# Kernel optimization log

Measured on AMD Instinct MI355X. Metric: run time of the kernel, lower is better.

Reference implementation:

```python
import jax, jax.numpy as jnp
import numpy as np

LN_EPS = 1e-5


def _sage_mean(x, Wl, bl, src, dst, ew, n_nodes):
    # lin_l then gather-weight-scatter mean: out[i] = mean_{j->i} ew * (x[j] @ Wl + bl)
    h = x @ Wl + bl                                  # [N, D]
    msg = h[src] * ew[:, None]                       # [E, D] gather + scale
    s = jax.ops.segment_sum(msg, dst, num_segments=n_nodes)          # [N, D]
    cnt = jax.ops.segment_sum(jnp.ones_like(ew), dst, num_segments=n_nodes)
    return s / jnp.maximum(cnt, 1.0)[:, None]


def _layernorm(x, gamma, beta):
    mu = jnp.mean(x, axis=-1, keepdims=True)
    var = jnp.var(x, axis=-1, keepdims=True)
    return (x - mu) * jax.lax.rsqrt(var + LN_EPS) * gamma + beta


def setup_inputs() -> dict:
    key = jax.random.key(0)
    ks = jax.random.split(key, 8)
    N, E, D = 50000, 800000, 128
    x = jax.random.normal(ks[0], (N, D), dtype=jnp.float32)
    edge_index = jax.random.randint(ks[1], (2, E), 0, N, dtype=jnp.int64)
    edge_weight = jax.random.uniform(ks[2], (E,), dtype=jnp.float32)
    sc = 1.0 / np.sqrt(D)
    Wl1 = jax.random.normal(ks[3], (D, D), dtype=jnp.float32) * sc
    bl1 = jnp.zeros((D,), dtype=jnp.float32)
    Wl2 = jax.random.normal(ks[4], (D, D), dtype=jnp.float32) * sc
    bl2 = jnp.zeros((D,), dtype=jnp.float32)
    gamma = jnp.ones((D,), dtype=jnp.float32)
    beta = jnp.zeros((D,), dtype=jnp.float32)
    return {"x": x, "edge_index": edge_index, "edge_weight": edge_weight,
            "Wl1": Wl1, "bl1": bl1, "Wl2": Wl2, "bl2": bl2,
            "gamma": gamma, "beta": beta}


def reference(x, edge_index, edge_weight, Wl1, bl1, Wl2, bl2, gamma, beta):
    N = x.shape[0]
    src, dst = edge_index[0], edge_index[1]
    # Layer 1: WeightedSAGEConv (no self-loops; update() returns aggr only)
    x1 = _sage_mean(x, Wl1, bl1, src, dst, edge_weight, N)
    # Layer 2: ResGraphConv — residual is Identity (in==out), add self-loops w=1
    loops = jnp.arange(N, dtype=edge_index.dtype)
    src2 = jnp.concatenate([src, loops])
    dst2 = jnp.concatenate([dst, loops])
    ew2 = jnp.concatenate([edge_weight, jnp.ones((N,), dtype=edge_weight.dtype)])
    out = _sage_mean(x1, Wl2, bl2, src2, dst2, ew2, N)
    out = _layernorm(out + x1, gamma, beta)
    return jax.nn.gelu(out, approximate=False)
```

## Files before the change

### kernel.cpp

```cpp
#include <hip/hip_runtime.h>
#include <math.h>

#define DF 128
#define NPB 256
#define EPB 4096
#define EPBA 2048
#define CAP 7168

typedef __attribute__((ext_vector_type(8))) short bf16x8;
typedef __attribute__((ext_vector_type(4))) float f32x4;

__device__ __forceinline__ float bf2f(uint u) {
    union { uint i; float f; } v; v.i = u << 16; return v.f;
}
__device__ __forceinline__ uint f2bf(float f) {
    union { float f; uint i; } v; v.f = f;
    return (v.i + 0x7fffu + ((v.i >> 16) & 1u)) >> 16;
}


__global__ void prep_k(const float* __restrict__ x, uint* __restrict__ xb, int n4,
                       const float* __restrict__ W1, const float* __restrict__ W2,
                       uint* __restrict__ Wt1, uint* __restrict__ Wt2,
                       const int* __restrict__ dst, int* __restrict__ bhist, int E,
                       int cvtxB) {
    __shared__ int lh[256];
    int b = blockIdx.x;
    int t = threadIdx.x;
    if (b < cvtxB) {
        int i = b * 256 + t;
        if (i < n4) {
            float4 v = ((const float4*)x)[i];
            uint2 o;
            o.x = f2bf(v.x) | (f2bf(v.y) << 16);
            o.y = f2bf(v.z) | (f2bf(v.w) << 16);
            ((uint2*)xb)[i] = o;
        }
    } else if (b < cvtxB + 64) {
        int i = (b - cvtxB) * 256 + t;
        const float* W = (i < 8192) ? W1 : W2;
        uint* Wt = (i < 8192) ? Wt1 : Wt2;
        int j = i & 8191;
        int n = j >> 6, kk = j & 63;
        Wt[n * 64 + kk] = f2bf(W[(2 * kk) * DF + n]) | (f2bf(W[(2 * kk + 1) * DF + n]) << 16);
    } else {
        int hb = b - cvtxB - 64;
        int base = hb * EPB;
        lh[t] = 0;
        __syncthreads();
#pragma unroll
        for (int k = 0; k < EPB / 256; ++k) {
            int i = base + k * 256 + t;
            if (i < E) atomicAdd(&lh[dst[i] >> 8], 1);
        }
        __syncthreads();
        bhist[hb * 256 + t] = lh[t];
    }
}

__global__ void bscan_k(const int* __restrict__ bhist, int histB,
                        int* __restrict__ bkoff, int* __restrict__ gcur) {
    int t = threadIdx.x;
    int v = 0;
#pragma unroll 4
    for (int hb = 0; hb < histB; ++hb) v += bhist[hb * 256 + t];
    __shared__ int sm[256];
    sm[t] = v;
    __syncthreads();
    for (int off = 1; off < 256; off <<= 1) {
        int u = (t >= off) ? sm[t - off] : 0;
        __syncthreads();
        sm[t] += u;
        __syncthreads();
    }
    int ex = sm[t] - v;
    bkoff[t] = ex;
    gcur[t] = ex;
    if (t == 255) bkoff[256] = sm[255];
}

__global__ __launch_bounds__(256) void passA_k(
    const int* __restrict__ src, const int* __restrict__ dst,
    const float* __restrict__ ew, int* __restrict__ gcur,
    uint2* __restrict__ stage, int E) {
    __shared__ int lhist[256];
    __shared__ int lscan[256];
    __shared__ int lcur[256];
    __shared__ int gbase[256];
    __shared__ int lbk[EPBA];
    __shared__ uint2 img[EPBA];
    int t = threadIdx.x;
    int base = blockIdx.x * EPBA;
    int cnt = min(EPBA, E - base);
    lhist[t] = 0;
    __syncthreads();
    uint ps[EPBA / 256], pw[EPBA / 256];
    int pb[EPBA / 256];
#pragma unroll
    for (int k = 0; k < EPBA / 256; ++k) {
        int i = base + k * 256 + t;
        pb[k] = -1;
        if (i < E) {
            int d = dst[i];
            int bk = d >> 8;
            pb[k] = bk;
            ps[k] = (uint)src[i] | ((uint)(d & 255) << 23);
            pw[k] = __float_as_uint(ew[i]);
            atomicAdd(&lhist[bk], 1);
        }
    }
    __syncthreads();
    int v = lhist[t];
    lscan[t] = v;
    __syncthreads();
    for (int off = 1; off < 256; off <<= 1) {
        int u = (t >= off) ? lscan[t - off] : 0;
        __syncthreads();
        lscan[t] += u;
        __syncthreads();
    }
    lcur[t] = lscan[t] - v;
    if (v > 0) gbase[t] = atomicAdd(&gcur[t], v);
    __syncthreads();
#pragma unroll
    for (int k = 0; k < EPBA / 256; ++k) {
        if (pb[k] >= 0) {
            int p = atomicAdd(&lcur[pb[k]], 1);
            img[p] = make_uint2(ps[k], pw[k]);
            lbk[p] = pb[k];
        }
    }
    __syncthreads();
    for (int i = t; i < cnt; i += 256) {
        int bk = lbk[i];
        stage[gbase[bk] + (i - (lscan[bk] - lhist[bk]))] = img[i];
    }
}

__global__ __launch_bounds__(256) void passB_k(
    const uint2* __restrict__ stage, const int* __restrict__ bkoff,
    int* __restrict__ rowptr, int* __restrict__ cursor,
    int2* __restrict__ adj, int N, int nbk) {
    __shared__ int lhist[256];
    __shared__ int lpre[256];
    __shared__ int lcur[256];
    __shared__ uint2 img[CAP];
    int t = threadIdx.x;
    int b = blockIdx.x;
    int nb0 = b * NPB;
    int nn = min(NPB, N - nb0);
    int ebase = bkoff[b];
    int ecnt = bkoff[b + 1] - ebase;
    lhist[t] = 0;
    __syncthreads();
    for (int i = t; i < ecnt; i += 256) {
        uint2 e = stage[ebase + i];
        atomicAdd(&lhist[(e.x >> 23) & 255], 1);
    }
    __syncthreads();
    int v = lhist[t];
    lpre[t] = v;
    __syncthreads();
    for (int off = 1; off < 256; off <<= 1) {
        int u = (t >= off) ? lpre[t - off] : 0;
        __syncthreads();
        lpre[t] += u;
        __syncthreads();
    }
    int myoff = lpre[t] - v;
    lcur[t] = myoff;
    if (t < nn) {
        rowptr[nb0 + t] = ebase + myoff;
        cursor[nb0 + t] = ebase + myoff;
    }
    if (b == nbk - 1 && t == 0) rowptr[N] = ebase + ecnt;
    __syncthreads();
    if (ecnt <= CAP) {
        for (int i = t; i < ecnt; i += 256) {
            uint2 e = stage[ebase + i];
            int p = atomicAdd(&lcur[(e.x >> 23) & 255], 1);
            img[p] = make_uint2(e.x & 0x7fffffu, e.y);
        }
        __syncthreads();
        for (int i = t; i < ecnt; i += 256) {
            uint2 e = img[i];
            adj[ebase + i] = make_int2((int)e.x, (int)e.y);
        }
    } else {
        for (int i = t; i < ecnt; i += 256) {
            uint2 e = stage[ebase + i];
            int dl = (e.x >> 23) & 255;
            int p = atomicAdd(&cursor[nb0 + dl], 1);
            adj[p] = make_int2((int)(e.x & 0x7fffffu), (int)e.y);
        }
    }
}


__global__ void histn_k(const int* __restrict__ dst, int* __restrict__ cnt, int E) {
    int i = blockIdx.x * blockDim.x + threadIdx.x;
    if (i < E) atomicAdd(&cnt[dst[i]], 1);
}

__global__ void partial_k(const int* __restrict__ cnt, int* __restrict__ bsum, int N) {
    int t = threadIdx.x, b = blockIdx.x;
    int base = b * 1024 + t * 4;
    int s = 0;
    if (base + 4 <= N) {
        int4 v = *(const int4*)(cnt + base);
        s = v.x + v.y + v.z + v.w;
    } else {
        for (int j = 0; j < 4; ++j)
            if (base + j < N) s += cnt[base + j];
    }
    __shared__ int sm[256];
    sm[t] = s;
    __syncthreads();
    for (int off = 128; off > 0; off >>= 1) {
        if (t < off) sm[t] += sm[t + off];
        __syncthreads();
    }
    if (t == 0) bsum[b] = sm[0];
}

__global__ void scanb_k(const int* __restrict__ bsum, int* __restrict__ boff,
                        int* __restrict__ rowptr, int nb, int N) {
    int t = threadIdx.x;
    int v = (t < nb) ? bsum[t] : 0;
    __shared__ int sm[256];
    sm[t] = v;
    __syncthreads();
    for (int off = 1; off < 256; off <<= 1) {
        int u = (t >= off) ? sm[t - off] : 0;
        __syncthreads();
        sm[t] += u;
        __syncthreads();
    }
    if (t < nb) boff[t] = sm[t] - v;
    if (t == 255) rowptr[N] = sm[255];
}

__global__ void rowfill_k(const int* __restrict__ cnt, const int* __restrict__ boff,
                          int* __restrict__ rowptr, int* __restrict__ cursor, int N) {
    int t = threadIdx.x, b = blockIdx.x;
    int base = b * 1024 + t * 4;
    int c0 = 0, c1 = 0, c2 = 0, c3 = 0;
    if (base + 4 <= N) {
        int4 v = *(const int4*)(cnt + base);
        c0 = v.x; c1 = v.y; c2 = v.z; c3 = v.w;
    } else {
        if (base + 0 < N) c0 = cnt[base + 0];
        if (base + 1 < N) c1 = cnt[base + 1];
        if (base + 2 < N) c2 = cnt[base + 2];
        if (base + 3 < N) c3 = cnt[base + 3];
    }
    int s = c0 + c1 + c2 + c3;
    __shared__ int sm[256];
    sm[t] = s;
    __syncthreads();
    for (int off = 1; off < 256; off <<= 1) {
        int u = (t >= off) ? sm[t - off] : 0;
        __syncthreads();
        sm[t] += u;
        __syncthreads();
    }
    int run = boff[b] + sm[t] - s;
    if (base + 0 < N) { rowptr[base + 0] = run; cursor[base + 0] = run; run += c0; }
    if (base + 1 < N) { rowptr[base + 1] = run; cursor[base + 1] = run; run += c1; }
    if (base + 2 < N) { rowptr[base + 2] = run; cursor[base + 2] = run; run += c2; }
    if (base + 3 < N) { rowptr[base + 3] = run; cursor[base + 3] = run; run += c3; }
}

__global__ void fill_k(const int* __restrict__ src, const int* __restrict__ dst,
                       const float* __restrict__ ew, int* __restrict__ cursor,
                       int2* __restrict__ adj, int E) {
    int i = blockIdx.x * blockDim.x + threadIdx.x;
    if (i < E) {
        int p = atomicAdd(&cursor[dst[i]], 1);
        int2 e;
        e.x = src[i];
        e.y = __float_as_int(ew[i]);
        adj[p] = e;
    }
}


template <int SELF>
__global__ void agg_k(const uint4* __restrict__ xb4, const int* __restrict__ rowptr,
                      const int2* __restrict__ adj, uint4* __restrict__ aggb4,
                      float* __restrict__ sumew, int N) {
    int wid = (blockIdx.x * blockDim.x + threadIdx.x) >> 6;
    int lane = threadIdx.x & 63;
    if (wid >= N) return;
    int g = lane >> 4;
    int c = lane & 15;
    int lo = rowptr[wid], hi = rowptr[wid + 1];
    float a0 = 0.f, a1 = 0.f, a2 = 0.f, a3 = 0.f;
    float a4 = 0.f, a5 = 0.f, a6 = 0.f, a7 = 0.f, ws = 0.f;
    if (SELF && g == 0) {
        uint4 v = xb4[(size_t)wid * 16 + c];
        a0 = bf2f(v.x & 0xffffu); a1 = bf2f(v.x >> 16);
        a2 = bf2f(v.y & 0xffffu); a3 = bf2f(v.y >> 16);
        a4 = bf2f(v.z & 0xffffu); a5 = bf2f(v.z >> 16);
        a6 = bf2f(v.w & 0xffffu); a7 = bf2f(v.w >> 16);
    }
#define FMA8(V, W)                                                     \
    do {                                                               \
        a0 += (W) * bf2f((V).x & 0xffffu); a1 += (W) * bf2f((V).x >> 16); \
        a2 += (W) * bf2f((V).y & 0xffffu); a3 += (W) * bf2f((V).y >> 16); \
        a4 += (W) * bf2f((V).z & 0xffffu); a5 += (W) * bf2f((V).z >> 16); \
        a6 += (W) * bf2f((V).w & 0xffffu); a7 += (W) * bf2f((V).w >> 16); \
    } while (0)
    for (int base = lo; base < hi; base += 64) {
        int p = base + lane;
        int sidx = 0; float wv = 0.f;
        if (p < hi) {
            int2 e = adj[p];
            sidx = e.x;
            wv = __int_as_float(e.y);
        }
        ws += wv;
        int cnt = min(hi - base, 64);
        int j = 0;
        for (; j + 16 <= cnt; j += 16) {
            int s0 = __shfl(sidx, j + g),      s1 = __shfl(sidx, j + 4 + g);
            int s2 = __shfl(sidx, j + 8 + g),  s3 = __shfl(sidx, j + 12 + g);
            float w0 = __shfl(wv, j + g),      w1 = __shfl(wv, j + 4 + g);
            float w2 = __shfl(wv, j + 8 + g),  w3 = __shfl(wv, j + 12 + g);
            uint4 v0 = xb4[(size_t)s0 * 16 + c];
            uint4 v1 = xb4[(size_t)s1 * 16 + c];
            uint4 v2 = xb4[(size_t)s2 * 16 + c];
            uint4 v3 = xb4[(size_t)s3 * 16 + c];
            FMA8(v0, w0); FMA8(v1, w1); FMA8(v2, w2); FMA8(v3, w3);
        }
        for (; j < cnt; j += 4) {
            int s0 = __shfl(sidx, j + g);
            float w0 = __shfl(wv, j + g);
            uint4 v0 = xb4[(size_t)s0 * 16 + c];
            FMA8(v0, w0);
        }
    }
#undef FMA8
    a0 += __shfl_xor(a0, 16); a0 += __shfl_xor(a0, 32);
    a1 += __shfl_xor(a1, 16); a1 += __shfl_xor(a1, 32);
    a2 += __shfl_xor(a2, 16); a2 += __shfl_xor(a2, 32);
    a3 += __shfl_xor(a3, 16); a3 += __shfl_xor(a3, 32);
    a4 += __shfl_xor(a4, 16); a4 += __shfl_xor(a4, 32);
    a5 += __shfl_xor(a5, 16); a5 += __shfl_xor(a5, 32);
    a6 += __shfl_xor(a6, 16); a6 += __shfl_xor(a6, 32);
    a7 += __shfl_xor(a7, 16); a7 += __shfl_xor(a7, 32);
    if (!SELF) {
        ws += __shfl_xor(ws, 1);
        ws += __shfl_xor(ws, 2);
        ws += __shfl_xor(ws, 4);
        ws += __shfl_xor(ws, 8);
        ws += __shfl_xor(ws, 16);
        ws += __shfl_xor(ws, 32);
        if (lane == 0) sumew[wid] = ws;
    }
    float inv = SELF ? 1.0f / (float)(hi - lo + 1)
                     : 1.0f / fmaxf((float)(hi - lo), 1.0f);
    if (g == 0) {
        uint4 o;
        o.x = f2bf(a0 * inv) | (f2bf(a1 * inv) << 16);
        o.y = f2bf(a2 * inv) | (f2bf(a3 * inv) << 16);
        o.z = f2bf(a4 * inv) | (f2bf(a5 * inv) << 16);
        o.w = f2bf(a6 * inv) | (f2bf(a7 * inv) << 16);
        aggb4[(size_t)wid * 16 + c] = o;
    }
}


__global__ __launch_bounds__(256) void mm1_k(
    const ushort* __restrict__ aggb, const ushort* __restrict__ Wt,
    const float* __restrict__ bl, const float* __restrict__ sumew,
    const int* __restrict__ rowptr, ushort* __restrict__ x1b, int N) {
    int lane = threadIdx.x & 63;
    int strip = blockIdx.x * 4 + (threadIdx.x >> 6);
    int nstrips = (N + 15) >> 4;
    if (strip >= nstrips) return;
    int row0 = strip << 4;
    int arow = row0 + (lane & 15);
    if (arow >= N) arow = N - 1;
    int kg = (lane >> 4) << 3;
    int bcol = lane & 15;

    bf16x8 af[4];
#pragma unroll
    for (int kc = 0; kc < 4; ++kc)
        af[kc] = *(const bf16x8*)(aggb + (size_t)arow * DF + kc * 32 + kg);

    f32x4 acc[8];
#pragma unroll
    for (int nt = 0; nt < 8; ++nt) {
        f32x4 a = {0.f, 0.f, 0.f, 0.f};
#pragma unroll
        for (int kc = 0; kc < 4; ++kc) {
            bf16x8 bf = *(const bf16x8*)(Wt + (size_t)(nt * 16 + bcol) * DF + kc * 32 + kg);
            a = __builtin_amdgcn_mfma_f32_16x16x32_bf16(af[kc], bf, a, 0, 0, 0);
        }
        acc[nt] = a;
    }

#pragma unroll
    for (int r = 0; r < 4; ++r) {
        int R = row0 + ((lane >> 4) << 2) + r;
        if (R >= N) continue;
        int deg = rowptr[R + 1] - rowptr[R];
        float wb = sumew[R] / fmaxf((float)deg, 1.0f);
#pragma unroll
        for (int nt = 0; nt < 8; ++nt) {
            int col = nt * 16 + bcol;
            x1b[(size_t)R * DF + col] = (ushort)f2bf(acc[nt][r] + bl[col] * wb);
        }
    }
}

__device__ __forceinline__ float gelu_exact(float v) {
    return 0.5f * v * (1.0f + erff(v * 0.70710678118654752440f));
}

__global__ __launch_bounds__(256) void mm2_k(
    const ushort* __restrict__ aggb, const ushort* __restrict__ Wt,
    const float* __restrict__ bl, const float* __restrict__ sumew,
    const int* __restrict__ rowptr, const ushort* __restrict__ x1b,
    const float* __restrict__ gamma, const float* __restrict__ beta,
    float* __restrict__ out, int N) {
    int lane = threadIdx.x & 63;
    int strip = blockIdx.x * 4 + (threadIdx.x >> 6);
    int nstrips = (N + 15) >> 4;
    if (strip >= nstrips) return;
    int row0 = strip << 4;
    int arow = row0 + (lane & 15);
    if (arow >= N) arow = N - 1;
    int kg = (lane >> 4) << 3;
    int bcol = lane & 15;

    bf16x8 af[4];
#pragma unroll
    for (int kc = 0; kc < 4; ++kc)
        af[kc] = *(const bf16x8*)(aggb + (size_t)arow * DF + kc * 32 + kg);

    f32x4 acc[8];
#pragma unroll
    for (int nt = 0; nt < 8; ++nt) {
        f32x4 a = {0.f, 0.f, 0.f, 0.f};
#pragma unroll
        for (int kc = 0; kc < 4; ++kc) {
            bf16x8 bf = *(const bf16x8*)(Wt + (size_t)(nt * 16 + bcol) * DF + kc * 32 + kg);
            a = __builtin_amdgcn_mfma_f32_16x16x32_bf16(af[kc], bf, a, 0, 0, 0);
        }
        acc[nt] = a;
    }

#pragma unroll
    for (int r = 0; r < 4; ++r) {
        int R = row0 + ((lane >> 4) << 2) + r;
        if (R >= N) continue;
        int deg = rowptr[R + 1] - rowptr[R];
        float wb = (sumew[R] + 1.0f) / (float)(deg + 1);
        float pre[8];
        float s = 0.f;
#pragma unroll
        for (int nt = 0; nt < 8; ++nt) {
            int col = nt * 16 + bcol;
            pre[nt] = acc[nt][r] + bl[col] * wb + bf2f(x1b[(size_t)R * DF + col]);
            s += pre[nt];
        }
        s += __shfl_xor(s, 1);
        s += __shfl_xor(s, 2);
        s += __shfl_xor(s, 4);
        s += __shfl_xor(s, 8);
        float mu = s * (1.0f / 128.0f);
        float vs = 0.f;
#pragma unroll
        for (int nt = 0; nt < 8; ++nt) {
            float d = pre[nt] - mu;
            vs += d * d;
        }
        vs += __shfl_xor(vs, 1);
        vs += __shfl_xor(vs, 2);
        vs += __shfl_xor(vs, 4);
        vs += __shfl_xor(vs, 8);
        float rstd = rsqrtf(vs * (1.0f / 128.0f) + 1e-5f);
#pragma unroll
        for (int nt = 0; nt < 8; ++nt) {
            int col = nt * 16 + bcol;
            float y = (pre[nt] - mu) * rstd * gamma[col] + beta[col];
            out[(size_t)R * DF + col] = gelu_exact(y);
        }
    }
}


extern "C" void kernel_launch(void* const* d_in, const int* in_sizes, int n_in,
                              void* d_out, int out_size, void* d_ws, size_t ws_size,
                              hipStream_t stream) {
    const float* x     = (const float*)d_in[0];
    const int*   ei    = (const int*)d_in[1];
    const float* ew    = (const float*)d_in[2];
    const float* Wl1   = (const float*)d_in[3];
    const float* bl1   = (const float*)d_in[4];
    const float* Wl2   = (const float*)d_in[5];
    const float* bl2   = (const float*)d_in[6];
    const float* gamma = (const float*)d_in[7];
    const float* beta  = (const float*)d_in[8];
    float* out = (float*)d_out;

    int N = in_sizes[0] / DF;
    int E = in_sizes[2];
    const int* src = ei;
    const int* dst = ei + E;

    char* ws = (char*)d_ws;
    size_t off = 0;
    auto alloc = [&](size_t bytes) -> void* {
        void* p = ws + off;
        off += (bytes + 255) & ~(size_t)255;
        return p;
    };
    int histB = (E + EPB - 1) / EPB;
    float*  sumew   = (float*)alloc((size_t)N * 4);
    int*    rowptr  = (int*)alloc((size_t)(N + 1) * 4);
    int*    cursor  = (int*)alloc((size_t)N * 4);
    int*    bhist   = (int*)alloc((size_t)histB * 256 * 4);
    int*    bkoff   = (int*)alloc(1040);
    int*    gcur    = (int*)alloc(1024);
    int*    bsum    = (int*)alloc(1024);
    int*    boff    = (int*)alloc(1024);
    int2*   adj     = (int2*)alloc((size_t)E * 8);
    uint2*  stage   = (uint2*)alloc((size_t)E * 8);
    uint*   xb      = (uint*)alloc((size_t)N * DF * 2);
    uint*   aggb    = (uint*)alloc((size_t)N * DF * 2);
    ushort* x1b     = (ushort*)alloc((size_t)N * DF * 2);
    uint*   Wt1     = (uint*)alloc((size_t)DF * DF * 2);
    uint*   Wt2     = (uint*)alloc((size_t)DF * DF * 2);
    int*    cnt     = (int*)alloc((size_t)N * 4);

    int nbk = (N + NPB - 1) / NPB;
    int n4 = N * DF / 4;
    int cvtxB = (n4 + 255) / 256;

    if (nbk <= 256) {
        hipLaunchKernelGGL(prep_k, dim3(cvtxB + 64 + histB), dim3(256), 0, stream,
                           x, xb, n4, Wl1, Wl2, Wt1, Wt2, dst, bhist, E, cvtxB);
        hipLaunchKernelGGL(bscan_k, dim3(1), dim3(256), 0, stream, bhist, histB, bkoff, gcur);
        int aB = (E + EPBA - 1) / EPBA;
        hipLaunchKernelGGL(passA_k, dim3(aB), dim3(256), 0, stream, src, dst, ew, gcur, stage, E);
        hipLaunchKernelGGL(passB_k, dim3(nbk), dim3(256), 0, stream,
                           stage, bkoff, rowptr, cursor, adj, N, nbk);
    } else {
        hipMemsetAsync(cnt, 0, (size_t)N * 4, stream);
        hipLaunchKernelGGL(prep_k, dim3(cvtxB + 64), dim3(256), 0, stream,
                           x, xb, n4, Wl1, Wl2, Wt1, Wt2, dst, bhist, 0, cvtxB);
        int eb = (E + 255) / 256;
        hipLaunchKernelGGL(histn_k, dim3(eb), dim3(256), 0, stream, dst, cnt, E);
        int nb_scan = (N + 1023) / 1024;
        hipLaunchKernelGGL(partial_k, dim3(nb_scan), dim3(256), 0, stream, cnt, bsum, N);
        hipLaunchKernelGGL(scanb_k, dim3(1), dim3(256), 0, stream, bsum, boff, rowptr, nb_scan, N);
        hipLaunchKernelGGL(rowfill_k, dim3(nb_scan), dim3(256), 0, stream, cnt, boff, rowptr, cursor, N);
        hipLaunchKernelGGL(fill_k, dim3(eb), dim3(256), 0, stream, src, dst, ew, cursor, adj, E);
    }

    int nb = (N * 64 + 255) / 256;
    int nstrips = (N + 15) / 16;
    int mb = (nstrips + 3) / 4;

    hipLaunchKernelGGL(agg_k<0>, dim3(nb), dim3(256), 0, stream,
                       (const uint4*)xb, rowptr, adj, (uint4*)aggb, sumew, N);
    hipLaunchKernelGGL(mm1_k, dim3(mb), dim3(256), 0, stream,
                       (const ushort*)aggb, (const ushort*)Wt1, bl1, sumew, rowptr, x1b, N);
    hipLaunchKernelGGL(agg_k<1>, dim3(nb), dim3(256), 0, stream,
                       (const uint4*)x1b, rowptr, adj, (uint4*)aggb, sumew, N);
    hipLaunchKernelGGL(mm2_k, dim3(mb), dim3(256), 0, stream,
                       (const ushort*)aggb, (const ushort*)Wt2, bl2, sumew, rowptr, x1b, gamma, beta, out, N);
}
```

Baseline: 169.5 us.

## Fuse neighbor aggregation with MFMA projection into one kernel per layer

Merges the aggregation and matmul kernels for each layer into a single kernel. Each block aggregates 16 nodes into shared memory, then one wave runs the MFMA projection plus bias, and for layer 2 the residual, layernorm and GELU. This drops the intermediate aggregate buffer round-trip, the sumew array and two launches. In exchange, three of four waves sit idle during the matmul phase and Wt is reloaded per 16-row block.

```diff
diff --git a/kernel.cpp b/kernel.cpp
--- a/kernel.cpp
+++ b/kernel.cpp
@@ -79,6 +79,7 @@
     if (t == 255) bkoff[256] = sm[255];
 }
 
+
 __global__ __launch_bounds__(256) void passA_k(
     const int* __restrict__ src, const int* __restrict__ dst,
     const float* __restrict__ ew, int* __restrict__ gcur,
@@ -285,110 +286,122 @@
 }
 
 
+__device__ __forceinline__ float gelu_exact(float v) {
+    return 0.5f * v * (1.0f + erff(v * 0.70710678118654752440f));
+}
+
 template <int SELF>
-__global__ void agg_k(const uint4* __restrict__ xb4, const int* __restrict__ rowptr,
-                      const int2* __restrict__ adj, uint4* __restrict__ aggb4,
-                      float* __restrict__ sumew, int N) {
-    int wid = (blockIdx.x * blockDim.x + threadIdx.x) >> 6;
-    int lane = threadIdx.x & 63;
-    if (wid >= N) return;
-    int g = lane >> 4;
-    int c = lane & 15;
-    int lo = rowptr[wid], hi = rowptr[wid + 1];
-    float a0 = 0.f, a1 = 0.f, a2 = 0.f, a3 = 0.f;
-    float a4 = 0.f, a5 = 0.f, a6 = 0.f, a7 = 0.f, ws = 0.f;
-    if (SELF && g == 0) {
-        uint4 v = xb4[(size_t)wid * 16 + c];
-        a0 = bf2f(v.x & 0xffffu); a1 = bf2f(v.x >> 16);
-        a2 = bf2f(v.y & 0xffffu); a3 = bf2f(v.y >> 16);
-        a4 = bf2f(v.z & 0xffffu); a5 = bf2f(v.z >> 16);
-        a6 = bf2f(v.w & 0xffffu); a7 = bf2f(v.w >> 16);
-    }
-#define FMA8(V, W)                                                     \
-    do {                                                               \
+__global__ __launch_bounds__(256) void aggmm_k(
+    const uint4* __restrict__ xin4, const int* __restrict__ rowptr,
+    const int2* __restrict__ adj, const ushort* __restrict__ Wt,
+    const float* __restrict__ bl, const float* __restrict__ gamma,
+    const float* __restrict__ beta, ushort* __restrict__ outb,
+    float* __restrict__ outf, int N) {
+    __shared__ __align__(16) ushort rows[16][136];
+    __shared__ float wbs[16];
+    int t = threadIdx.x;
+    int wv = t >> 6;
+    int lane = t & 63;
+    int row0 = blockIdx.x << 4;
+    int g = lane >> 4, c = lane & 15;
+
+#define FMA8(V, W)                                                        \
+    do {                                                                  \
         a0 += (W) * bf2f((V).x & 0xffffu); a1 += (W) * bf2f((V).x >> 16); \
         a2 += (W) * bf2f((V).y & 0xffffu); a3 += (W) * bf2f((V).y >> 16); \
         a4 += (W) * bf2f((V).z & 0xffffu); a5 += (W) * bf2f((V).z >> 16); \
         a6 += (W) * bf2f((V).w & 0xffffu); a7 += (W) * bf2f((V).w >> 16); \
     } while (0)
-    for (int base = lo; base < hi; base += 64) {
-        int p = base + lane;
-        int sidx = 0; float wv = 0.f;
-        if (p < hi) {
-            int2 e = adj[p];
-            sidx = e.x;
-            wv = __int_as_float(e.y);
-        }
-        ws += wv;
-        int cnt = min(hi - base, 64);
-        int j = 0;
-        for (; j + 16 <= cnt; j += 16) {
-            int s0 = __shfl(sidx, j + g),      s1 = __shfl(sidx, j + 4 + g);
-            int s2 = __shfl(sidx, j + 8 + g),  s3 = __shfl(sidx, j + 12 + g);
-            float w0 = __shfl(wv, j + g),      w1 = __shfl(wv, j + 4 + g);
-            float w2 = __shfl(wv, j + 8 + g),  w3 = __shfl(wv, j + 12 + g);
-            uint4 v0 = xb4[(size_t)s0 * 16 + c];
-            uint4 v1 = xb4[(size_t)s1 * 16 + c];
-            uint4 v2 = xb4[(size_t)s2 * 16 + c];
-            uint4 v3 = xb4[(size_t)s3 * 16 + c];
-            FMA8(v0, w0); FMA8(v1, w1); FMA8(v2, w2); FMA8(v3, w3);
-        }
-        for (; j < cnt; j += 4) {
-            int s0 = __shfl(sidx, j + g);
-            float w0 = __shfl(wv, j + g);
-            uint4 v0 = xb4[(size_t)s0 * 16 + c];
-            FMA8(v0, w0);
-        }
-    }
-#undef FMA8
-    a0 += __shfl_xor(a0, 16); a0 += __shfl_xor(a0, 32);
-    a1 += __shfl_xor(a1, 16); a1 += __shfl_xor(a1, 32);
-    a2 += __shfl_xor(a2, 16); a2 += __shfl_xor(a2, 32);
-    a3 += __shfl_xor(a3, 16); a3 += __shfl_xor(a3, 32);
-    a4 += __shfl_xor(a4, 16); a4 += __shfl_xor(a4, 32);
-    a5 += __shfl_xor(a5, 16); a5 += __shfl_xor(a5, 32);
-    a6 += __shfl_xor(a6, 16); a6 += __shfl_xor(a6, 32);
-    a7 += __shfl_xor(a7, 16); a7 += __shfl_xor(a7, 32);
-    if (!SELF) {
+
+    for (int q = 0; q < 4; ++q) {
+        int i = wv + q * 4;
+        int node = row0 + i;
+        float a0 = 0.f, a1 = 0.f, a2 = 0.f, a3 = 0.f;
+        float a4 = 0.f, a5 = 0.f, a6 = 0.f, a7 = 0.f, ws = 0.f;
+        int lo = 0, hi = 0;
+        if (node < N) {
+            lo = rowptr[node];
+            hi = rowptr[node + 1];
+            if (SELF && g == 0) {
+                uint4 v = xin4[(size_t)node * 16 + c];
+                a0 = bf2f(v.x & 0xffffu); a1 = bf2f(v.x >> 16);
+                a2 = bf2f(v.y & 0xffffu); a3 = bf2f(v.y >> 16);
+                a4 = bf2f(v.z & 0xffffu); a5 = bf2f(v.z >> 16);
+                a6 = bf2f(v.w & 0xffffu); a7 = bf2f(v.w >> 16);
+            }
+        }
+        for (int base = lo; base < hi; base += 64) {
+            int p = base + lane;
+            int sidx = 0; float wv2 = 0.f;
+            if (p < hi) {
+                int2 e = adj[p];
+                sidx = e.x;
+                wv2 = __int_as_float(e.y);
+            }
+            ws += wv2;
+            int cnt = min(hi - base, 64);
+            int j = 0;
+            for (; j + 16 <= cnt; j += 16) {
+                int s0 = __shfl(sidx, j + g),     s1 = __shfl(sidx, j + 4 + g);
+                int s2 = __shfl(sidx, j + 8 + g), s3 = __shfl(sidx, j + 12 + g);
+                float w0 = __shfl(wv2, j + g),     w1 = __shfl(wv2, j + 4 + g);
+                float w2 = __shfl(wv2, j + 8 + g), w3 = __shfl(wv2, j + 12 + g);
+                uint4 v0 = xin4[(size_t)s0 * 16 + c];
+                uint4 v1 = xin4[(size_t)s1 * 16 + c];
+                uint4 v2 = xin4[(size_t)s2 * 16 + c];
+                uint4 v3 = xin4[(size_t)s3 * 16 + c];
+                FMA8(v0, w0); FMA8(v1, w1); FMA8(v2, w2); FMA8(v3, w3);
+            }
+            for (; j < cnt; j += 4) {
+                int s0 = __shfl(sidx, j + g);
+                float w0 = __shfl(wv2, j + g);
+                uint4 v0 = xin4[(size_t)s0 * 16 + c];
+                FMA8(v0, w0);
+            }
+        }
+        a0 += __shfl_xor(a0, 16); a0 += __shfl_xor(a0, 32);
+        a1 += __shfl_xor(a1, 16); a1 += __shfl_xor(a1, 32);
+        a2 += __shfl_xor(a2, 16); a2 += __shfl_xor(a2, 32);
+        a3 += __shfl_xor(a3, 16); a3 += __shfl_xor(a3, 32);
+        a4 += __shfl_xor(a4, 16); a4 += __shfl_xor(a4, 32);
+        a5 += __shfl_xor(a5, 16); a5 += __shfl_xor(a5, 32);
+        a6 += __shfl_xor(a6, 16); a6 += __shfl_xor(a6, 32);
+        a7 += __shfl_xor(a7, 16); a7 += __shfl_xor(a7, 32);
         ws += __shfl_xor(ws, 1);
         ws += __shfl_xor(ws, 2);
         ws += __shfl_xor(ws, 4);
         ws += __shfl_xor(ws, 8);
         ws += __shfl_xor(ws, 16);
         ws += __shfl_xor(ws, 32);
-        if (lane == 0) sumew[wid] = ws;
-    }
-    float inv = SELF ? 1.0f / (float)(hi - lo + 1)
-                     : 1.0f / fmaxf((float)(hi - lo), 1.0f);
-    if (g == 0) {
-        uint4 o;
-        o.x = f2bf(a0 * inv) | (f2bf(a1 * inv) << 16);
-        o.y = f2bf(a2 * inv) | (f2bf(a3 * inv) << 16);
-        o.z = f2bf(a4 * inv) | (f2bf(a5 * inv) << 16);
-        o.w = f2bf(a6 * inv) | (f2bf(a7 * inv) << 16);
-        aggb4[(size_t)wid * 16 + c] = o;
-    }
-}
-
-
-__global__ __launch_bounds__(256) void mm1_k(
-    const ushort* __restrict__ aggb, const ushort* __restrict__ Wt,
-    const float* __restrict__ bl, const float* __restrict__ sumew,
-    const int* __restrict__ rowptr, ushort* __restrict__ x1b, int N) {
-    int lane = threadIdx.x & 63;
-    int strip = blockIdx.x * 4 + (threadIdx.x >> 6);
-    int nstrips = (N + 15) >> 4;
-    if (strip >= nstrips) return;
-    int row0 = strip << 4;
-    int arow = row0 + (lane & 15);
-    if (arow >= N) arow = N - 1;
-    int kg = (lane >> 4) << 3;
-    int bcol = lane & 15;
-
+        int deg = hi - lo;
+        float inv, wb;
+        if (SELF) {
+            inv = 1.0f / (float)(deg + 1);
+            wb = (ws + 1.0f) * inv;
+        } else {
+            float dd = fmaxf((float)deg, 1.0f);
+            inv = 1.0f / dd;
+            wb = ws / dd;
+        }
+        if (g == 0) {
+            uint4 o;
+            o.x = f2bf(a0 * inv) | (f2bf(a1 * inv) << 16);
+            o.y = f2bf(a2 * inv) | (f2bf(a3 * inv) << 16);
+            o.z = f2bf(a4 * inv) | (f2bf(a5 * inv) << 16);
+            o.w = f2bf(a6 * inv) | (f2bf(a7 * inv) << 16);
+            *reinterpret_cast<uint4*>(&rows[i][c * 8]) = o;
+            if (c == 0) wbs[i] = wb;
+        }
+    }
+#undef FMA8
+    __syncthreads();
+    if (wv != 0) return;
+
+    int kg = g << 3;
     bf16x8 af[4];
 #pragma unroll
     for (int kc = 0; kc < 4; ++kc)
-        af[kc] = *(const bf16x8*)(aggb + (size_t)arow * DF + kc * 32 + kg);
+        af[kc] = *(const bf16x8*)&rows[c][kc * 32 + kg];
 
     f32x4 acc[8];
 #pragma unroll
@@ -396,98 +409,56 @@
         f32x4 a = {0.f, 0.f, 0.f, 0.f};
 #pragma unroll
         for (int kc = 0; kc < 4; ++kc) {
-            bf16x8 bf = *(const bf16x8*)(Wt + (size_t)(nt * 16 + bcol) * DF + kc * 32 + kg);
+            bf16x8 bf = *(const bf16x8*)(Wt + (size_t)(nt * 16 + c) * DF + kc * 32 + kg);
             a = __builtin_amdgcn_mfma_f32_16x16x32_bf16(af[kc], bf, a, 0, 0, 0);
         }
         acc[nt] = a;
     }
 
+    const ushort* xin_s = (const ushort*)xin4;
 #pragma unroll
     for (int r = 0; r < 4; ++r) {
-        int R = row0 + ((lane >> 4) << 2) + r;
+        int i = g * 4 + r;
+        int R = row0 + i;
         if (R >= N) continue;
-        int deg = rowptr[R + 1] - rowptr[R];
-        float wb = sumew[R] / fmaxf((float)deg, 1.0f);
-#pragma unroll
-        for (int nt = 0; nt < 8; ++nt) {
-            int col = nt * 16 + bcol;
-            x1b[(size_t)R * DF + col] = (ushort)f2bf(acc[nt][r] + bl[col] * wb);
-        }
-    }
-}
-
-__device__ __forceinline__ float gelu_exact(float v) {
-    return 0.5f * v * (1.0f + erff(v * 0.70710678118654752440f));
-}
-
-__global__ __launch_bounds__(256) void mm2_k(
-    const ushort* __restrict__ aggb, const ushort* __restrict__ Wt,
-    const float* __restrict__ bl, const float* __restrict__ sumew,
-    const int* __restrict__ rowptr, const ushort* __restrict__ x1b,
-    const float* __restrict__ gamma, const float* __restrict__ beta,
-    float* __restrict__ out, int N) {
-    int lane = threadIdx.x & 63;
-    int strip = blockIdx.x * 4 + (threadIdx.x >> 6);
-    int nstrips = (N + 15) >> 4;
-    if (strip >= nstrips) return;
-    int row0 = strip << 4;
-    int arow = row0 + (lane & 15);
-    if (arow >= N) arow = N - 1;
-    int kg = (lane >> 4) << 3;
-    int bcol = lane & 15;
-
-    bf16x8 af[4];
-#pragma unroll
-    for (int kc = 0; kc < 4; ++kc)
-        af[kc] = *(const bf16x8*)(aggb + (size_t)arow * DF + kc * 32 + kg);
-
-    f32x4 acc[8];
-#pragma unroll
-    for (int nt = 0; nt < 8; ++nt) {
-        f32x4 a = {0.f, 0.f, 0.f, 0.f};
-#pragma unroll
-        for (int kc = 0; kc < 4; ++kc) {
-            bf16x8 bf = *(const bf16x8*)(Wt + (size_t)(nt * 16 + bcol) * DF + kc * 32 + kg);
-            a = __builtin_amdgcn_mfma_f32_16x16x32_bf16(af[kc], bf, a, 0, 0, 0);
-        }
-        acc[nt] = a;
-    }
-
-#pragma unroll
-    for (int r = 0; r < 4; ++r) {
-        int R = row0 + ((lane >> 4) << 2) + r;
-        if (R >= N) continue;
-        int deg = rowptr[R + 1] - rowptr[R];
-        float wb = (sumew[R] + 1.0f) / (float)(deg + 1);
-        float pre[8];
-        float s = 0.f;
-#pragma unroll
-        for (int nt = 0; nt < 8; ++nt) {
-            int col = nt * 16 + bcol;
-            pre[nt] = acc[nt][r] + bl[col] * wb + bf2f(x1b[(size_t)R * DF + col]);
-            s += pre[nt];
-        }
-        s += __shfl_xor(s, 1);
-        s += __shfl_xor(s, 2);
-        s += __shfl_xor(s, 4);
-        s += __shfl_xor(s, 8);
-        float mu = s * (1.0f / 128.0f);
-        float vs = 0.f;
-#pragma unroll
-        for (int nt = 0; nt < 8; ++nt) {
-            float d = pre[nt] - mu;
-            vs += d * d;
-        }
-        vs += __shfl_xor(vs, 1);
-        vs += __shfl_xor(vs, 2);
-        vs += __shfl_xor(vs, 4);
-        vs += __shfl_xor(vs, 8);
-        float rstd = rsqrtf(vs * (1.0f / 128.0f) + 1e-5f);
-#pragma unroll
-        for (int nt = 0; nt < 8; ++nt) {
-            int col = nt * 16 + bcol;
-            float y = (pre[nt] - mu) * rstd * gamma[col] + beta[col];
-            out[(size_t)R * DF + col] = gelu_exact(y);
+        float wb = wbs[i];
+        if (!SELF) {
+#pragma unroll
+            for (int nt = 0; nt < 8; ++nt) {
+                int col = nt * 16 + c;
+                outb[(size_t)R * DF + col] = (ushort)f2bf(acc[nt][r] + bl[col] * wb);
+            }
+        } else {
+            float pre[8];
+            float s = 0.f;
+#pragma unroll
+            for (int nt = 0; nt < 8; ++nt) {
+                int col = nt * 16 + c;
+                pre[nt] = acc[nt][r] + bl[col] * wb + bf2f(xin_s[(size_t)R * DF + col]);
+                s += pre[nt];
+            }
+            s += __shfl_xor(s, 1);
+            s += __shfl_xor(s, 2);
+            s += __shfl_xor(s, 4);
+            s += __shfl_xor(s, 8);
+            float mu = s * (1.0f / 128.0f);
+            float vs = 0.f;
+#pragma unroll
+            for (int nt = 0; nt < 8; ++nt) {
+                float d = pre[nt] - mu;
+                vs += d * d;
+            }
+            vs += __shfl_xor(vs, 1);
+            vs += __shfl_xor(vs, 2);
+            vs += __shfl_xor(vs, 4);
+            vs += __shfl_xor(vs, 8);
+            float rstd = rsqrtf(vs * (1.0f / 128.0f) + 1e-5f);
+#pragma unroll
+            for (int nt = 0; nt < 8; ++nt) {
+                int col = nt * 16 + c;
+                float y = (pre[nt] - mu) * rstd * gamma[col] + beta[col];
+                outf[(size_t)R * DF + col] = gelu_exact(y);
+            }
         }
     }
 }
@@ -520,7 +491,6 @@
         return p;
     };
     int histB = (E + EPB - 1) / EPB;
-    float*  sumew   = (float*)alloc((size_t)N * 4);
     int*    rowptr  = (int*)alloc((size_t)(N + 1) * 4);
     int*    cursor  = (int*)alloc((size_t)N * 4);
     int*    bhist   = (int*)alloc((size_t)histB * 256 * 4);
@@ -531,7 +501,6 @@
     int2*   adj     = (int2*)alloc((size_t)E * 8);
     uint2*  stage   = (uint2*)alloc((size_t)E * 8);
     uint*   xb      = (uint*)alloc((size_t)N * DF * 2);
-    uint*   aggb    = (uint*)alloc((size_t)N * DF * 2);
     ushort* x1b     = (ushort*)alloc((size_t)N * DF * 2);
     uint*   Wt1     = (uint*)alloc((size_t)DF * DF * 2);
     uint*   Wt2     = (uint*)alloc((size_t)DF * DF * 2);
@@ -562,16 +531,11 @@
         hipLaunchKernelGGL(fill_k, dim3(eb), dim3(256), 0, stream, src, dst, ew, cursor, adj, E);
     }
 
-    int nb = (N * 64 + 255) / 256;
     int nstrips = (N + 15) / 16;
-    int mb = (nstrips + 3) / 4;
-
-    hipLaunchKernelGGL(agg_k<0>, dim3(nb), dim3(256), 0, stream,
-                       (const uint4*)xb, rowptr, adj, (uint4*)aggb, sumew, N);
-    hipLaunchKernelGGL(mm1_k, dim3(mb), dim3(256), 0, stream,
-                       (const ushort*)aggb, (const ushort*)Wt1, bl1, sumew, rowptr, x1b, N);
-    hipLaunchKernelGGL(agg_k<1>, dim3(nb), dim3(256), 0, stream,
-                       (const uint4*)x1b, rowptr, adj, (uint4*)aggb, sumew, N);
-    hipLaunchKernelGGL(mm2_k, dim3(mb), dim3(256), 0, stream,
-                       (const ushort*)aggb, (const ushort*)Wt2, bl2, sumew, rowptr, x1b, gamma, beta, out, N);
-}
+    hipLaunchKernelGGL(aggmm_k<0>, dim3(nstrips), dim3(256), 0, stream,
+                       (const uint4*)xb, rowptr, adj, (const ushort*)Wt1, bl1,
+                       gamma, beta, x1b, (float*)nullptr, N);
+    hipLaunchKernelGGL(aggmm_k<1>, dim3(nstrips), dim3(256), 0, stream,
+                       (const uint4*)x1b, rowptr, adj, (const ushort*)Wt2, bl2,
+                       gamma, beta, (ushort*)nullptr, out, N);
+}
```

Result: no change. 167.9 us, median of 2 (-0.9%).
